# Optimization experiments

Measured on AMD Instinct MI355X. Metric: run time of the kernel, lower is better.

## Reference

```python
import jax, jax.numpy as jnp
import numpy as np
from jax import lax

B, S, I, H = 4096, 512, 1, 50


def setup_inputs() -> dict:
    key = jax.random.key(0)
    ks = jax.random.split(key, 7)
    return {
        "x": jax.random.normal(ks[0], (B, S, I), dtype=jnp.float32),
        "W_ih": jax.random.normal(ks[1], (4 * H, I), dtype=jnp.float32) * 0.1,
        "W_hh": jax.random.normal(ks[2], (4 * H, H), dtype=jnp.float32) * 0.1,
        "b_ih": jax.random.normal(ks[3], (4 * H,), dtype=jnp.float32) * 0.1,
        "b_hh": jax.random.normal(ks[4], (4 * H,), dtype=jnp.float32) * 0.1,
        "W_fc": jax.random.normal(ks[5], (1, H), dtype=jnp.float32) * 0.1,
        "b_fc": jax.random.normal(ks[6], (1,), dtype=jnp.float32) * 0.1,
    }


def reference(x, W_ih, W_hh, b_ih, b_hh, W_fc, b_fc):
    # Single-layer LSTM (PyTorch gate order i, f, g, o), batch_first input.
    b = b_ih + b_hh  # [4H]
    # Precompute input projections for all timesteps: [B,S,4H] -> scan over S
    x_proj = jnp.einsum("bsi,gi->bsg", x, W_ih) + b  # g = 4H
    xs = jnp.swapaxes(x_proj, 0, 1)  # [S, B, 4H]

    h0 = jnp.zeros((x.shape[0], W_hh.shape[1]), dtype=x.dtype)
    c0 = jnp.zeros_like(h0)

    def step(carry, xp):
        h, c = carry
        z = xp + h @ W_hh.T  # [B, 4H]
        i, f, g, o = jnp.split(z, 4, axis=-1)
        i = jax.nn.sigmoid(i)
        f = jax.nn.sigmoid(f)
        g = jnp.tanh(g)
        o = jax.nn.sigmoid(o)
        c = f * c + i * g
        h = o * jnp.tanh(c)
        return (h, c), None

    (h_last, _), _ = lax.scan(step, (h0, c0), xs)
    out = h_last @ W_fc.T + b_fc  # [B, 1]
    return jax.nn.sigmoid(out)
```

## Files before the change

kernel.cpp:

```cpp
#include <hip/hip_runtime.h>

#define S_LEN 512
#define HID   50
#define NB    16
#define NTHR  832

typedef _Float16 f16x8 __attribute__((ext_vector_type(8)));
typedef float    f32x4 __attribute__((ext_vector_type(4)));

#define LOG2E 1.44269504088896340736f

__device__ __forceinline__ float ex2(float a) {
#if __has_builtin(__builtin_amdgcn_exp2f)
    return __builtin_amdgcn_exp2f(a);
#else
    return __expf(0.69314718055994531f * a);
#endif
}
__device__ __forceinline__ float rcpf(float a) {
#if __has_builtin(__builtin_amdgcn_rcpf)
    return __builtin_amdgcn_rcpf(a);
#else
    return 1.0f / a;
#endif
}
__device__ __forceinline__ float sig_s(float a)  { return rcpf(1.0f + ex2(a)); }
__device__ __forceinline__ float tanh_s(float a) { return fmaf(-2.0f, rcpf(1.0f + ex2(a)), 1.0f); }

__device__ __forceinline__ int hIdx(int b, int u) {
    return b * 64 + ((((u >> 3) ^ (b & 7))) << 3) + (u & 7);
}

__global__ __launch_bounds__(NTHR, 1) void lstm_mfma_kernel(
    const float* __restrict__ x,
    const float* __restrict__ W_ih,
    const float* __restrict__ W_hh,
    const float* __restrict__ b_ih,
    const float* __restrict__ b_hh,
    const float* __restrict__ W_fc,
    const float* __restrict__ b_fc,
    float* __restrict__ out)
{
    const int blk  = blockIdx.x;
    const int tid  = threadIdx.x;
    const int wave = tid >> 6;
    const int lane = tid & 63;
    const int bcol = lane & 15;
    const int grp  = lane >> 4;

    __shared__ __align__(16) float    x_lds[S_LEN][NB];
    __shared__ __align__(16) _Float16 h_lds[2][NB * 64];

    for (int i = tid; i < 2 * NB * 64; i += NTHR)
        (&h_lds[0][0])[i] = (_Float16)0.0f;
    __syncthreads();

    if (tid < 512) {
        const int bb  = tid >> 5;
        const int ss0 = tid & 31;
        const float* xrow = x + (size_t)(blk * NB + bb) * S_LEN;
        #pragma unroll
        for (int i = 0; i < 16; ++i) {
            const int s = ss0 + 32 * i;
            x_lds[s][bb] = xrow[s];
        }
    }
    if (tid < NB) {
        h_lds[0][hIdx(tid, 50)] = (_Float16)x[(size_t)(blk * NB + tid) * S_LEN];
        h_lds[0][hIdx(tid, 51)] = (_Float16)1.0f;
        h_lds[1][hIdx(tid, 51)] = (_Float16)1.0f;
    }

    f16x8 af0, af1;
    {
        const int prow = 16 * wave + (lane & 15);
        const int ua = prow >> 2, ga = prow & 3;
        const float sc = (ga == 2) ? (2.0f * LOG2E) : (-LOG2E);
        const int orow = ga * HID + ua;
        #pragma unroll
        for (int kc = 0; kc < 2; ++kc) {
            f16x8 fr;
            #pragma unroll
            for (int e = 0; e < 8; ++e) {
                const int k = 32 * kc + 8 * grp + e;
                float wv = 0.0f;
                if (ua < HID) {
                    if (k < HID)       wv = W_hh[orow * HID + k];
                    else if (k == 50)  wv = W_ih[orow];
                    else if (k == 51)  wv = b_ih[orow] + b_hh[orow];
                }
                fr[e] = (_Float16)(sc * wv);
            }
            if (kc == 0) af0 = fr; else af1 = fr;
        }
    }

    const int u   = 4 * wave + grp;
    const bool wr = (u < HID);
    const int widx = hIdx(bcol, u < 64 ? u : 0);
    const int off0 = bcol * 64 + ((grp ^ (bcol & 7)) << 3);
    const int off1 = bcol * 64 + (((4 + grp) ^ (bcol & 7)) << 3);
    const bool xfeed = (wave == 12) && (lane < NB);

    float cst = 0.0f;

    __syncthreads();

    for (int s = 0; s < S_LEN; ++s) {
        const _Float16* hcur = h_lds[s & 1];
        _Float16*       hnxt = h_lds[(s & 1) ^ 1];

        const f16x8 bfr0 = *reinterpret_cast<const f16x8*>(hcur + off0);
        const f16x8 bfr1 = *reinterpret_cast<const f16x8*>(hcur + off1);

        f32x4 acc = {0.0f, 0.0f, 0.0f, 0.0f};
        acc = __builtin_amdgcn_mfma_f32_16x16x32_f16(af0, bfr0, acc, 0, 0, 0);
        acc = __builtin_amdgcn_mfma_f32_16x16x32_f16(af1, bfr1, acc, 0, 0, 0);

        const float ig = sig_s(acc[0]);
        const float fg = sig_s(acc[1]);
        const float gg = tanh_s(acc[2]);
        const float og = sig_s(acc[3]);
        cst = fmaf(fg, cst, ig * gg);
        const float hv = og * tanh_s(cst * (2.0f * LOG2E));
        if (wr) hnxt[widx] = (_Float16)hv;

        if (xfeed && s + 1 < S_LEN)
            hnxt[hIdx(lane, 50)] = (_Float16)x_lds[s + 1][lane];

        __syncthreads();
    }

    if (tid < NB) {
        const _Float16* hf = h_lds[0];
        float sum = b_fc[0];
        for (int uu = 0; uu < HID; ++uu)
            sum += W_fc[uu] * (float)hf[hIdx(tid, uu)];
        out[blk * NB + tid] = 1.0f / (1.0f + __expf(-sum));
    }
}

extern "C" void kernel_launch(void* const* d_in, const int* in_sizes, int n_in,
                              void* d_out, int out_size, void* d_ws, size_t ws_size,
                              hipStream_t stream) {
    const float* x    = (const float*)d_in[0];
    const float* W_ih = (const float*)d_in[1];
    const float* W_hh = (const float*)d_in[2];
    const float* b_ih = (const float*)d_in[3];
    const float* b_hh = (const float*)d_in[4];
    const float* W_fc = (const float*)d_in[5];
    const float* b_fc = (const float*)d_in[6];
    float* out = (float*)d_out;

    lstm_mfma_kernel<<<4096 / NB, NTHR, 0, stream>>>(x, W_ih, W_hh, b_ih, b_hh,
                                                     W_fc, b_fc, out);
}
```

Before: 283.1 us.

## Consolidate 13 waves into 4 waves each processing multiple gate tiles

Shrinks the block from 13 waves to 4, with each wave now computing 3 or 4 of the 13 MFMA gate tiles serially and keeping its own cell-state registers per tile. The aim is to cut the cost of the per-timestep __syncthreads barrier across many waves and to fit more blocks per CU, so that independent batch groups overlap. In exchange each wave does more serial MFMA and transcendental work per step, which lengthens the critical path of the recurrence. The x staging loop is remapped to cover all 512 timesteps with 256 threads.

```diff
diff --git a/kernel.cpp b/kernel.cpp
--- a/kernel.cpp
+++ b/kernel.cpp
@@ -3,7 +3,7 @@
 #define S_LEN 512
 #define HID   50
 #define NB    16
-#define NTHR  832
+#define NTHR  256
 
 typedef _Float16 f16x8 __attribute__((ext_vector_type(8)));
 typedef float    f32x4 __attribute__((ext_vector_type(4)));
@@ -55,13 +55,13 @@
         (&h_lds[0][0])[i] = (_Float16)0.0f;
     __syncthreads();
 
-    if (tid < 512) {
-        const int bb  = tid >> 5;
-        const int ss0 = tid & 31;
+    {
+        const int bb  = tid >> 4;
+        const int ss0 = tid & 15;
         const float* xrow = x + (size_t)(blk * NB + bb) * S_LEN;
         #pragma unroll
-        for (int i = 0; i < 16; ++i) {
-            const int s = ss0 + 32 * i;
+        for (int i = 0; i < 32; ++i) {
+            const int s = ss0 + 16 * i;
             x_lds[s][bb] = xrow[s];
         }
     }
@@ -71,9 +71,12 @@
         h_lds[1][hIdx(tid, 51)] = (_Float16)1.0f;
     }
 
-    f16x8 af0, af1;
-    {
-        const int prow = 16 * wave + (lane & 15);
+    const int t0  = (wave == 0) ? 0 : (wave == 1) ? 4 : (wave == 2) ? 7 : 10;
+    const int ntl = (wave == 0) ? 4 : 3;
+
+    f16x8 afA[2], afB[2], afC[2], afD[2];
+    auto load_tile = [&](int t, bool active, f16x8 (&af)[2]) __attribute__((always_inline)) {
+        const int prow = 16 * t + (lane & 15);
         const int ua = prow >> 2, ga = prow & 3;
         const float sc = (ga == 2) ? (2.0f * LOG2E) : (-LOG2E);
         const int orow = ga * HID + ua;
@@ -84,25 +87,32 @@
             for (int e = 0; e < 8; ++e) {
                 const int k = 32 * kc + 8 * grp + e;
                 float wv = 0.0f;
-                if (ua < HID) {
+                if (active && ua < HID) {
                     if (k < HID)       wv = W_hh[orow * HID + k];
                     else if (k == 50)  wv = W_ih[orow];
                     else if (k == 51)  wv = b_ih[orow] + b_hh[orow];
                 }
                 fr[e] = (_Float16)(sc * wv);
             }
-            if (kc == 0) af0 = fr; else af1 = fr;
+            af[kc] = fr;
         }
-    }
+    };
+    load_tile(t0 + 0, true,      afA);
+    load_tile(t0 + 1, true,      afB);
+    load_tile(t0 + 2, true,      afC);
+    load_tile(t0 + 3, ntl == 4,  afD);
 
-    const int u   = 4 * wave + grp;
-    const bool wr = (u < HID);
-    const int widx = hIdx(bcol, u < 64 ? u : 0);
+    const int uA = 4 * (t0 + 0) + grp, uB = 4 * (t0 + 1) + grp;
+    const int uC = 4 * (t0 + 2) + grp, uD = 4 * (t0 + 3) + grp;
+    const bool wA = (uA < HID), wB = (uB < HID);
+    const bool wC = (uC < HID), wD = (uD < HID) && (ntl == 4);
+    const int iA = hIdx(bcol, uA < 64 ? uA : 0), iB = hIdx(bcol, uB < 64 ? uB : 0);
+    const int iC = hIdx(bcol, uC < 64 ? uC : 0), iD = hIdx(bcol, uD < 64 ? uD : 0);
     const int off0 = bcol * 64 + ((grp ^ (bcol & 7)) << 3);
     const int off1 = bcol * 64 + (((4 + grp) ^ (bcol & 7)) << 3);
-    const bool xfeed = (wave == 12) && (lane < NB);
+    const bool xfeed = (wave == 3) && (lane < NB);
 
-    float cst = 0.0f;
+    float cstA = 0.0f, cstB = 0.0f, cstC = 0.0f, cstD = 0.0f;
 
     __syncthreads();
 
@@ -113,17 +123,23 @@
         const f16x8 bfr0 = *reinterpret_cast<const f16x8*>(hcur + off0);
         const f16x8 bfr1 = *reinterpret_cast<const f16x8*>(hcur + off1);
 
-        f32x4 acc = {0.0f, 0.0f, 0.0f, 0.0f};
-        acc = __builtin_amdgcn_mfma_f32_16x16x32_f16(af0, bfr0, acc, 0, 0, 0);
-        acc = __builtin_amdgcn_mfma_f32_16x16x32_f16(af1, bfr1, acc, 0, 0, 0);
-
-        const float ig = sig_s(acc[0]);
-        const float fg = sig_s(acc[1]);
-        const float gg = tanh_s(acc[2]);
-        const float og = sig_s(acc[3]);
-        cst = fmaf(fg, cst, ig * gg);
-        const float hv = og * tanh_s(cst * (2.0f * LOG2E));
-        if (wr) hnxt[widx] = (_Float16)hv;
+        auto do_tile = [&](const f16x8 (&af)[2], float& cst,
+                           int widx, bool wr) __attribute__((always_inline)) {
+            f32x4 acc = {0.0f, 0.0f, 0.0f, 0.0f};
+            acc = __builtin_amdgcn_mfma_f32_16x16x32_f16(af[0], bfr0, acc, 0, 0, 0);
+            acc = __builtin_amdgcn_mfma_f32_16x16x32_f16(af[1], bfr1, acc, 0, 0, 0);
+            const float ig = sig_s(acc[0]);
+            const float fg = sig_s(acc[1]);
+            const float gg = tanh_s(acc[2]);
+            const float og = sig_s(acc[3]);
+            cst = fmaf(fg, cst, ig * gg);
+            const float hv = og * tanh_s(cst * (2.0f * LOG2E));
+            if (wr) hnxt[widx] = (_Float16)hv;
+        };
+        do_tile(afA, cstA, iA, wA);
+        do_tile(afB, cstB, iB, wB);
+        do_tile(afC, cstC, iC, wC);
+        if (ntl == 4) do_tile(afD, cstD, iD, wD);
 
         if (xfeed && s + 1 < S_LEN)
             hnxt[hIdx(lane, 50)] = (_Float16)x_lds[s + 1][lane];
```

After: 301.5 us. 6.5% more time.
